# Optimization experiments

Hardware: AMD Instinct MI355X
Metric: run time of the kernel (lower is better)

Reference implementation:

```python
import jax, jax.numpy as jnp
import numpy as np

B, T, DIN, DOUT = 64, 512, 512, 512


def setup_inputs() -> dict:
    key = jax.random.key(0)
    ks = jax.random.split(key, 8)
    s_in = 1.0 / np.sqrt(DIN)
    s_h = 1.0 / np.sqrt(DOUT)
    return {
        "X": jax.random.normal(ks[0], (B, T, DIN), dtype=jnp.float32),
        "mask": jnp.ones((B, T), dtype=jnp.int32),
        "W_z": jax.random.normal(ks[1], (DIN, DOUT), dtype=jnp.float32) * s_in,
        "U_z": jax.random.normal(ks[2], (DOUT, DOUT), dtype=jnp.float32) * s_h,
        "b_z": jnp.zeros((DOUT,), dtype=jnp.float32),
        "W_r": jax.random.normal(ks[3], (DIN, DOUT), dtype=jnp.float32) * s_in,
        "U_r": jax.random.normal(ks[4], (DOUT, DOUT), dtype=jnp.float32) * s_h,
        "b_r": jnp.zeros((DOUT,), dtype=jnp.float32),
        "W_h": jax.random.normal(ks[5], (DIN, DOUT), dtype=jnp.float32) * s_in,
        "U_h": jax.random.normal(ks[6], (DOUT, DOUT), dtype=jnp.float32) * s_h,
        "b_h": jnp.zeros((DOUT,), dtype=jnp.float32),
    }


def reference(X, mask, W_z, U_z, b_z, W_r, U_r, b_r, W_h, U_h, b_h):
    # Precompute input projections for all timesteps (as the original does),
    # then scan the recurrence over time. return_sequences=False -> final h.
    # time-major: [T, B, DOUT]
    x_z = jnp.einsum('btd,dh->tbh', X, W_z) + b_z
    x_r = jnp.einsum('btd,dh->tbh', X, W_r) + b_r
    x_h = jnp.einsum('btd,dh->tbh', X, W_h) + b_h
    m = mask.T[:, :, None]  # [T, B, 1]

    def step(h, inp):
        xz_t, xr_t, xh_t, m_t = inp
        z = jax.nn.sigmoid(xz_t + h @ U_z)
        r = jax.nn.sigmoid(xr_t + h @ U_r)
        hh = jnp.tanh(xh_t + (r * h) @ U_h)
        h_new = z * h + (1.0 - z) * hh
        h_new = jnp.where(m_t > 0, h_new, h)  # masked steps keep previous state
        return h_new, None

    h0 = jnp.zeros((X.shape[0], U_z.shape[0]), dtype=X.dtype)
    h_final, _ = jax.lax.scan(step, h0, (x_z, x_r, x_h, m))
    return h_final
```

## Files before the change

### kernel.cpp

```cpp
#include <hip/hip_runtime.h>
#include <stdint.h>


#define GT    512
#define GDIN  512
#define GDOUT 512
#define NGRP  8
#define NSL   16
#define GROWS 8
#define COLS  32
#define NWAVE 8
#define KW    64
#define NWG   (NGRP * NSL)

#define OFF_HB    0
#define OFF_RHB   (2 * NGRP * GROWS * GDOUT)
#define OFF_HFL   (OFF_RHB + NGRP * GROWS * GDOUT)
#define FLSTR     4
#define FLGRP     (NSL * NWAVE * FLSTR)
#define OFF_RFL   (OFF_HFL + NGRP * FLGRP)
#define OFF_CNS   (OFF_RFL + NGRP * FLGRP)
#define INIT_DW   (OFF_CNS + 160)

typedef __attribute__((ext_vector_type(8))) short bf16x8;
typedef __attribute__((ext_vector_type(4))) float f32x4;
typedef __attribute__((ext_vector_type(4))) unsigned int u32x4;

__device__ __forceinline__ short f2bf(float f) {
  union { float f; uint32_t u; } v; v.f = f;
  uint32_t r = (v.u + 0x7FFFu + ((v.u >> 16) & 1u)) >> 16;
  return (short)(uint16_t)r;
}
__device__ __forceinline__ float bf2f(short s) {
  union { uint32_t u; float f; } v; v.u = ((uint32_t)(uint16_t)s) << 16;
  return v.f;
}
__device__ __forceinline__ uint32_t pack_hl(float v) {
  uint32_t t, o;
  asm("v_cvt_pk_bf16_f32 %0, %1, %1" : "=v"(t) : "v"(v));
  union { uint32_t u; float f; } hf; hf.u = t << 16;
  float d = v - hf.f;
  asm("v_cvt_pk_bf16_f32 %0, %1, %2" : "=v"(o) : "v"(d), "v"(v));
  return o;
}

__device__ __forceinline__ void st_sc1(uint32_t* p, uint32_t v) {
  asm volatile("global_store_dword %0, %1, off sc1" :: "v"(p), "v"(v) : "memory");
}
__device__ __forceinline__ void st_pl(uint32_t* p, uint32_t v) {
  asm volatile("global_store_dword %0, %1, off" :: "v"(p), "v"(v) : "memory");
}
__device__ __forceinline__ void vm_drain() {
  asm volatile("s_waitcnt vmcnt(0)" ::: "memory");
}
__device__ __forceinline__ void l1_inv() {
  asm volatile("buffer_inv sc1" ::: "memory");
}
__device__ __forceinline__ uint32_t ld_nt(const uint32_t* p) {
  uint32_t v;
  asm volatile("global_load_dword %0, %1, off nt\n\ts_waitcnt vmcnt(0)"
               : "=v"(v) : "v"(p) : "memory");
  return v;
}

__device__ __forceinline__ void slab4_issue(const uint32_t* base, u32x4 d[4],
                                            int fast) {
  if (fast) {
    asm volatile(
      "global_load_dwordx4 %0, %4, off nt\n\t"
      "global_load_dwordx4 %1, %4, off offset:16 nt\n\t"
      "global_load_dwordx4 %2, %4, off offset:128 nt\n\t"
      "global_load_dwordx4 %3, %4, off offset:144 nt"
      : "=&v"(d[0]), "=&v"(d[1]), "=&v"(d[2]), "=&v"(d[3])
      : "v"(base) : "memory");
  } else {
    asm volatile(
      "global_load_dwordx4 %0, %4, off sc1\n\t"
      "global_load_dwordx4 %1, %4, off offset:16 sc1\n\t"
      "global_load_dwordx4 %2, %4, off offset:128 sc1\n\t"
      "global_load_dwordx4 %3, %4, off offset:144 sc1"
      : "=&v"(d[0]), "=&v"(d[1]), "=&v"(d[2]), "=&v"(d[3])
      : "v"(base) : "memory");
  }
}
__device__ __forceinline__ void slab_wait() {
  asm volatile("s_waitcnt vmcnt(0)" ::: "memory");
  __builtin_amdgcn_sched_barrier(0);
}

__device__ __forceinline__ void wait16(const uint32_t* fbase, uint32_t tgt,
                                       int lane, int wv, int fast, int& budget) {
  if (budget <= 0) return;
  const int idx = lane & 15;
  const uint32_t* p = fbase +
      (size_t)(((2 * wv + (idx >> 3)) * NWAVE + (idx & 7)) * FLSTR);
  if (fast) {
    uint32_t v0, v1;
    asm volatile("global_load_dword %0, %1, off nt" : "=v"(v0) : "v"(p) : "memory");
    for (;;) {
      asm volatile("global_load_dword %0, %1, off nt" : "=v"(v1) : "v"(p) : "memory");
      asm volatile("s_waitcnt vmcnt(1)" ::: "memory");
      __builtin_amdgcn_sched_barrier(0);
      if (__all((int)(v0 >= tgt))) break;
      asm volatile("global_load_dword %0, %1, off nt" : "=v"(v0) : "v"(p) : "memory");
      asm volatile("s_waitcnt vmcnt(1)" ::: "memory");
      __builtin_amdgcn_sched_barrier(0);
      if (__all((int)(v1 >= tgt))) break;
      if ((budget -= 2) <= 0) break;
    }
    asm volatile("s_waitcnt vmcnt(0)" ::: "memory");
  } else {
    for (;;) {
      uint32_t v = __hip_atomic_load(p, __ATOMIC_RELAXED, __HIP_MEMORY_SCOPE_AGENT);
      if (__all((int)(v >= tgt))) break;
      if (--budget <= 0) break;
    }
  }
  asm volatile("" ::: "memory");
}

union U16x8 { uint32_t u[4]; bf16x8 v; };
__device__ __forceinline__ void mk_frags(const u32x4 A, const u32x4 B,
                                         bf16x8& hi, bf16x8& lo) {
  U16x8 h, l;
  h.u[0] = (A[0] >> 16) | (A[1] & 0xFFFF0000u);  l.u[0] = (A[0] & 0xFFFFu) | (A[1] << 16);
  h.u[1] = (A[2] >> 16) | (A[3] & 0xFFFF0000u);  l.u[1] = (A[2] & 0xFFFFu) | (A[3] << 16);
  h.u[2] = (B[0] >> 16) | (B[1] & 0xFFFF0000u);  l.u[2] = (B[0] & 0xFFFFu) | (B[1] << 16);
  h.u[3] = (B[2] >> 16) | (B[3] & 0xFFFF0000u);  l.u[3] = (B[2] & 0xFFFFu) | (B[3] << 16);
  hi = h.v; lo = l.v;
}
__device__ __forceinline__ bf16x8 cvt8(const f32x4 a, const f32x4 b) {
  U16x8 w;
  asm("v_cvt_pk_bf16_f32 %0, %1, %2" : "=v"(w.u[0]) : "v"(a[0]), "v"(a[1]));
  asm("v_cvt_pk_bf16_f32 %0, %1, %2" : "=v"(w.u[1]) : "v"(a[2]), "v"(a[3]));
  asm("v_cvt_pk_bf16_f32 %0, %1, %2" : "=v"(w.u[2]) : "v"(b[0]), "v"(b[1]));
  asm("v_cvt_pk_bf16_f32 %0, %1, %2" : "=v"(w.u[3]) : "v"(b[2]), "v"(b[3]));
  return w.v;
}

__global__ __launch_bounds__(512, 2)
void gru_fused(const float* __restrict__ X, const int* __restrict__ mask,
               const float* __restrict__ Wz, const float* __restrict__ Uz,
               const float* __restrict__ bz,
               const float* __restrict__ Wr, const float* __restrict__ Ur,
               const float* __restrict__ br,
               const float* __restrict__ Wh, const float* __restrict__ Uh,
               const float* __restrict__ bh,
               float* __restrict__ out, uint32_t* __restrict__ ws)
{
  const int tid   = threadIdx.x;
  const int wv    = tid >> 6;
  const int lane  = tid & 63;
  const int col16 = lane & 15;
  const int quad  = lane >> 4;
  const int row8  = lane & 7;

  uint32_t* cns = ws + OFF_CNS;
  __shared__ int s_mode, s_g, s_sl;
  if (tid == 0) {
    uint32_t xcc = 0;
    asm volatile("s_getreg_b32 %0, hwreg(HW_REG_XCC_ID)" : "=s"(xcc));
    xcc &= 7u;
    uint32_t slot = __hip_atomic_fetch_add(&cns[xcc], 1u, __ATOMIC_RELAXED,
                                           __HIP_MEMORY_SCOPE_AGENT);
    if (slot >= (uint32_t)NSL)
      __hip_atomic_fetch_add(&cns[9], 1u, __ATOMIC_RELAXED, __HIP_MEMORY_SCOPE_AGENT);
    __hip_atomic_fetch_add(&cns[8], 1u, __ATOMIC_RELEASE, __HIP_MEMORY_SCOPE_AGENT);
    uint32_t tv = 0; long sp = 0;
    do {
      tv = __hip_atomic_load(&cns[8], __ATOMIC_ACQUIRE, __HIP_MEMORY_SCOPE_AGENT);
    } while (tv < (uint32_t)NWG && ++sp < 2000000L);
    uint32_t bad = __hip_atomic_load(&cns[9], __ATOMIC_RELAXED, __HIP_MEMORY_SCOPE_AGENT);
    const int cok = (tv >= (uint32_t)NWG && bad == 0u);
    int g_, sl_, mode_ = 0;
    if (cok) {
      g_ = (int)xcc; sl_ = (int)slot;
      l1_inv();
      uint32_t* tok = cns + 16;
      st_pl(&tok[g_ * NSL + sl_], 1u);
      vm_drain();
      const uint32_t* np = &tok[g_ * NSL + ((sl_ + 1) & (NSL - 1))];
      int ok = 0;
      for (long i = 0; i < 300000L; ++i) {
        if (ld_nt(np) != 0u) { ok = 1; break; }
      }
      if (!ok)
        __hip_atomic_fetch_add(&cns[11], 1u, __ATOMIC_RELAXED, __HIP_MEMORY_SCOPE_AGENT);
      __hip_atomic_fetch_add(&cns[10], 1u, __ATOMIC_RELEASE, __HIP_MEMORY_SCOPE_AGENT);
      uint32_t tv2 = 0; sp = 0;
      do {
        tv2 = __hip_atomic_load(&cns[10], __ATOMIC_ACQUIRE, __HIP_MEMORY_SCOPE_AGENT);
      } while (tv2 < (uint32_t)NWG && ++sp < 2000000L);
      uint32_t fl = __hip_atomic_load(&cns[11], __ATOMIC_RELAXED, __HIP_MEMORY_SCOPE_AGENT);
      mode_ = (tv2 >= (uint32_t)NWG && fl == 0u) ? 1 : 0;
    } else {
      g_ = (int)(blockIdx.x & 7); sl_ = (int)(blockIdx.x >> 3);
    }
    s_mode = mode_; s_g = g_; s_sl = sl_;
  }
  __syncthreads();
  const int fast = __builtin_amdgcn_readfirstlane(s_mode);
  const int g    = __builtin_amdgcn_readfirstlane(s_g);
  const int sl   = __builtin_amdgcn_readfirstlane(s_sl);
  l1_inv();

  const int jb = sl * COLS;
  const int kb = wv * KW;

  uint32_t* hb  = ws + OFF_HB;
  uint32_t* rhb = ws + OFF_RHB;
  uint32_t* hfl = ws + OFF_HFL + (size_t)g * FLGRP;
  uint32_t* rfl = ws + OFF_RFL + (size_t)g * FLGRP;
  uint32_t* hfl_my = hfl + (size_t)(sl * NWAVE + wv) * FLSTR;
  uint32_t* rfl_my = rfl + (size_t)(sl * NWAVE + wv) * FLSTR;
  uint32_t* rhg = rhb + (size_t)g * (GROWS * GDOUT);
  const int slab_off = row8 * GDOUT + kb + quad * 8;

  __shared__ __align__(16) float scrA[2][NWAVE][2][GROWS][COLS];
  __shared__ __align__(16) float scrB[2][NWAVE][GROWS][COLS];

  bf16x8 uzh[2][2], uzl[2][2], urh[2][2], url[2][2], uhh[2][2], uhl[2][2];
  bf16x8 wzf[2][2], wrf[2][2], whf[2][2];
#pragma unroll
  for (int c = 0; c < 2; ++c) {
#pragma unroll
    for (int Tt = 0; Tt < 2; ++Tt) {
      const int k0 = kb + c * 32 + quad * 8;
      const int j  = jb + Tt * 16 + col16;
      bf16x8 t_uzh, t_uzl, t_urh, t_url, t_uhh, t_uhl, t_wz, t_wr, t_wh;
#pragma unroll
      for (int i = 0; i < 8; ++i) {
        const int idx = (k0 + i) * GDOUT + j;
        float u; short hi;
        u = Uz[idx]; hi = f2bf(u); t_uzh[i] = hi; t_uzl[i] = f2bf(u - bf2f(hi));
        u = Ur[idx]; hi = f2bf(u); t_urh[i] = hi; t_url[i] = f2bf(u - bf2f(hi));
        u = Uh[idx]; hi = f2bf(u); t_uhh[i] = hi; t_uhl[i] = f2bf(u - bf2f(hi));
        t_wz[i] = f2bf(Wz[idx]);
        t_wr[i] = f2bf(Wr[idx]);
        t_wh[i] = f2bf(Wh[idx]);
      }
      uzh[c][Tt] = t_uzh; uzl[c][Tt] = t_uzl; urh[c][Tt] = t_urh; url[c][Tt] = t_url;
      uhh[c][Tt] = t_uhh; uhl[c][Tt] = t_uhl;
      wzf[c][Tt] = t_wz;  wrf[c][Tt] = t_wr;  whf[c][Tt] = t_wh;
    }
  }

  const int ecol = lane & 31;
  const float bzv = bz[jb + ecol];
  const float brv = br[jb + ecol];
  const float bhv = bh[jb + ecol];
  const int b_ep = GROWS * g + wv;

  float hreg = 0.f;
  int budget = 4000000;

  f32x4 xpA[2], xpB[2]; int mkpre;
  {
    const float* xr = X + (size_t)(GROWS * g + row8) * GT * GDIN;
#pragma unroll
    for (int c = 0; c < 2; ++c) {
      const float* xp = xr + kb + c * 32 + quad * 8;
      xpA[c] = *(const f32x4*)xp;
      xpB[c] = *(const f32x4*)(xp + 4);
    }
    mkpre = mask[(size_t)b_ep * GT + 0];
  }

  for (int t = 0; t < GT; ++t) {
    const int par = t & 1;
    bf16x8 xa[2];
#pragma unroll
    for (int c = 0; c < 2; ++c) xa[c] = cvt8(xpA[c], xpB[c]);
    const int mk = mkpre;

    if (t) wait16(hfl, (uint32_t)t, lane, wv, fast, budget);
    const uint32_t* hsrc = hb + ((size_t)par * NGRP + g) * (GROWS * GDOUT) + slab_off;
    u32x4 hd[4];
    slab4_issue(hsrc, hd, fast);

    f32x4 ar[2]  = {{0,0,0,0},{0,0,0,0}}, ar2[2] = {{0,0,0,0},{0,0,0,0}};
#pragma unroll
    for (int c = 0; c < 2; ++c)
#pragma unroll
      for (int Tt = 0; Tt < 2; ++Tt)
        ar2[Tt] = __builtin_amdgcn_mfma_f32_16x16x32_bf16(xa[c], wrf[c][Tt], ar2[Tt], 0, 0, 0);
    slab_wait();

    bf16x8 hhi[2], hlo[2];
#pragma unroll
    for (int c = 0; c < 2; ++c) {
      mk_frags(hd[2 * c], hd[2 * c + 1], hhi[c], hlo[c]);
#pragma unroll
      for (int Tt = 0; Tt < 2; ++Tt) {
        ar[Tt]  = __builtin_amdgcn_mfma_f32_16x16x32_bf16(hhi[c], urh[c][Tt], ar[Tt],  0, 0, 0);
        ar2[Tt] = __builtin_amdgcn_mfma_f32_16x16x32_bf16(hlo[c], urh[c][Tt], ar2[Tt], 0, 0, 0);
        ar[Tt]  = __builtin_amdgcn_mfma_f32_16x16x32_bf16(hhi[c], url[c][Tt], ar[Tt],  0, 0, 0);
      }
    }

    if (quad < 2) {
#pragma unroll
      for (int Tt = 0; Tt < 2; ++Tt)
#pragma unroll
        for (int rr = 0; rr < 4; ++rr)
          scrA[par][wv][0][quad * 4 + rr][Tt * 16 + col16] = ar[Tt][rr] + ar2[Tt][rr];
    }
    __syncthreads();

    float rsum = 0.f;
#pragma unroll
    for (int w2 = 0; w2 < NWAVE; ++w2) rsum += scrA[par][w2][0][wv][ecol];
    const float rvl = 1.f / (1.f + __expf(-(rsum + brv)));
    if (lane < 32) {
      uint32_t* dst = rhg + (size_t)wv * GDOUT + jb + lane;
      const uint32_t pv = pack_hl(rvl * hreg);
      if (fast) st_pl(dst, pv); else st_sc1(dst, pv);
    }
    vm_drain();
    if (lane == 0) {
      if (fast) st_pl(rfl_my, (uint32_t)(t + 1)); else st_sc1(rfl_my, (uint32_t)(t + 1));
    }

    f32x4 az[2] = {{0,0,0,0},{0,0,0,0}}, az2[2] = {{0,0,0,0},{0,0,0,0}};
    f32x4 ah[2] = {{0,0,0,0},{0,0,0,0}};
#pragma unroll
    for (int c = 0; c < 2; ++c)
#pragma unroll
      for (int Tt = 0; Tt < 2; ++Tt) {
        az2[Tt] = __builtin_amdgcn_mfma_f32_16x16x32_bf16(xa[c], wzf[c][Tt], az2[Tt], 0, 0, 0);
        az[Tt]  = __builtin_amdgcn_mfma_f32_16x16x32_bf16(hhi[c], uzh[c][Tt], az[Tt],  0, 0, 0);
        az2[Tt] = __builtin_amdgcn_mfma_f32_16x16x32_bf16(hlo[c], uzh[c][Tt], az2[Tt], 0, 0, 0);
        az[Tt]  = __builtin_amdgcn_mfma_f32_16x16x32_bf16(hhi[c], uzl[c][Tt], az[Tt],  0, 0, 0);
        ah[Tt]  = __builtin_amdgcn_mfma_f32_16x16x32_bf16(xa[c],  whf[c][Tt], ah[Tt],  0, 0, 0);
      }
    if (quad < 2) {
#pragma unroll
      for (int Tt = 0; Tt < 2; ++Tt)
#pragma unroll
        for (int rr = 0; rr < 4; ++rr)
          scrA[par][wv][1][quad * 4 + rr][Tt * 16 + col16] = az[Tt][rr] + az2[Tt][rr];
    }
    __syncthreads();

    float zsum = 0.f;
#pragma unroll
    for (int w2 = 0; w2 < NWAVE; ++w2) zsum += scrA[par][w2][1][wv][ecol];
    const float zvl = 1.f / (1.f + __expf(-(zsum + bzv)));

    {
      const int tn = (t + 1 < GT) ? t + 1 : t;
      const float* xr = X + ((size_t)(GROWS * g + row8) * GT + tn) * GDIN;
#pragma unroll
      for (int c = 0; c < 2; ++c) {
        const float* xp = xr + kb + c * 32 + quad * 8;
        xpA[c] = *(const f32x4*)xp;
        xpB[c] = *(const f32x4*)(xp + 4);
      }
      mkpre = mask[(size_t)b_ep * GT + tn];
    }

    wait16(rfl, (uint32_t)(t + 1), lane, wv, fast, budget);
    u32x4 rd[4];
    slab4_issue(rhg + slab_off, rd, fast);
    slab_wait();

    f32x4 b1[2] = {{0,0,0,0},{0,0,0,0}}, b2[2] = {{0,0,0,0},{0,0,0,0}};
    f32x4 b3[2] = {{0,0,0,0},{0,0,0,0}};
#pragma unroll
    for (int c = 0; c < 2; ++c) {
      bf16x8 th, tl;
      mk_frags(rd[2 * c], rd[2 * c + 1], th, tl);
#pragma unroll
      for (int Tt = 0; Tt < 2; ++Tt) {
        b1[Tt] = __builtin_amdgcn_mfma_f32_16x16x32_bf16(th, uhh[c][Tt], b1[Tt], 0, 0, 0);
        b2[Tt] = __builtin_amdgcn_mfma_f32_16x16x32_bf16(tl, uhh[c][Tt], b2[Tt], 0, 0, 0);
        b3[Tt] = __builtin_amdgcn_mfma_f32_16x16x32_bf16(th, uhl[c][Tt], b3[Tt], 0, 0, 0);
      }
    }

    if (quad < 2) {
#pragma unroll
      for (int Tt = 0; Tt < 2; ++Tt)
#pragma unroll
        for (int rr = 0; rr < 4; ++rr)
          scrB[par][wv][quad * 4 + rr][Tt * 16 + col16] =
              ah[Tt][rr] + b1[Tt][rr] + b2[Tt][rr] + b3[Tt][rr];
    }
    __syncthreads();

    float hsum = 0.f;
#pragma unroll
    for (int w2 = 0; w2 < NWAVE; ++w2) hsum += scrB[par][w2][wv][ecol];
    const float pre = hsum + bhv;
    const float e  = __expf(2.f * pre);
    const float hh = 1.f - 2.f / (e + 1.f);
    float hn = zvl * hreg + (1.f - zvl) * hh;
    hn = (mk > 0) ? hn : hreg;
    hreg = hn;

    if (lane < 32) {
      uint32_t* hdst = hb + ((size_t)((t + 1) & 1) * NGRP + g) * (GROWS * GDOUT)
                         + (size_t)wv * GDOUT + jb + lane;
      const uint32_t pv = pack_hl(hn);
      if (fast) st_pl(hdst, pv); else st_sc1(hdst, pv);
      if (t == GT - 1) out[(size_t)b_ep * GDOUT + jb + lane] = hn;
    }
    vm_drain();
    if (lane == 0) {
      if (fast) st_pl(hfl_my, (uint32_t)(t + 1)); else st_sc1(hfl_my, (uint32_t)(t + 1));
    }
  }
}

extern "C" void kernel_launch(void* const* d_in, const int* in_sizes, int n_in,
                              void* d_out, int out_size, void* d_ws, size_t ws_size,
                              hipStream_t stream) {
  const float* X  = (const float*)d_in[0];
  const int* mask = (const int*)d_in[1];
  const float* Wz = (const float*)d_in[2];
  const float* Uz = (const float*)d_in[3];
  const float* bz = (const float*)d_in[4];
  const float* Wr = (const float*)d_in[5];
  const float* Ur = (const float*)d_in[6];
  const float* br = (const float*)d_in[7];
  const float* Wh = (const float*)d_in[8];
  const float* Uh = (const float*)d_in[9];
  const float* bh = (const float*)d_in[10];

  hipMemsetAsync(d_ws, 0, (size_t)INIT_DW * 4, stream);

  hipLaunchKernelGGL(gru_fused, dim3(NWG), dim3(512), 0, stream,
                     X, mask, Wz, Uz, bz, Wr, Ur, br, Wh, Uh, bh,
                     (float*)d_out, (uint32_t*)d_ws);
}
```

Measured before the change: 2.733 ms.

## Embed step tags in data words to replace separate flag synchronization

Removes the per-wave flag arrays and the vm_drain + flag store after each data publish. Instead, the low 2 bits of each packed bf16 hi/lo word carry a step tag (t mod 4), and consumers spin on the data slab itself until every word has the expected tag. This cuts one store, one full memory drain and one flag round trip per exchange on the serial recurrence critical path. In exchange, the low-order bf16 bits of each packed word are sacrificed (slight precision loss), and correctness now relies on per-dword store atomicity and on the tag never aliasing across the double-buffered slots.

```diff
diff --git a/kernel.cpp b/kernel.cpp
--- a/kernel.cpp
+++ b/kernel.cpp
@@ -15,11 +15,7 @@
 
 #define OFF_HB    0
 #define OFF_RHB   (2 * NGRP * GROWS * GDOUT)
-#define OFF_HFL   (OFF_RHB + NGRP * GROWS * GDOUT)
-#define FLSTR     4
-#define FLGRP     (NSL * NWAVE * FLSTR)
-#define OFF_RFL   (OFF_HFL + NGRP * FLGRP)
-#define OFF_CNS   (OFF_RFL + NGRP * FLGRP)
+#define OFF_CNS   (OFF_RHB + NGRP * GROWS * GDOUT)
 #define INIT_DW   (OFF_CNS + 160)
 
 typedef __attribute__((ext_vector_type(8))) short bf16x8;
@@ -59,6 +55,12 @@
 __device__ __forceinline__ uint32_t ld_nt(const uint32_t* p) {
   uint32_t v;
   asm volatile("global_load_dword %0, %1, off nt\n\ts_waitcnt vmcnt(0)"
+               : "=v"(v) : "v"(p) : "memory");
+  return v;
+}
+__device__ __forceinline__ uint32_t ld_sc1(const uint32_t* p) {
+  uint32_t v;
+  asm volatile("global_load_dword %0, %1, off sc1\n\ts_waitcnt vmcnt(0)"
                : "=v"(v) : "v"(p) : "memory");
   return v;
 }
@@ -88,35 +90,38 @@
   __builtin_amdgcn_sched_barrier(0);
 }
 
-__device__ __forceinline__ void wait16(const uint32_t* fbase, uint32_t tgt,
-                                       int lane, int wv, int fast, int& budget) {
+__device__ __forceinline__ void probe16(const uint32_t* kbase, uint32_t tg,
+                                        int lane, int fast, int& budget) {
   if (budget <= 0) return;
   const int idx = lane & 15;
-  const uint32_t* p = fbase +
-      (size_t)(((2 * wv + (idx >> 3)) * NWAVE + (idx & 7)) * FLSTR);
+  const uint32_t* p = kbase + (size_t)(idx & 7) * GDOUT + ((idx >> 3) << 5);
   if (fast) {
-    uint32_t v0, v1;
-    asm volatile("global_load_dword %0, %1, off nt" : "=v"(v0) : "v"(p) : "memory");
     for (;;) {
-      asm volatile("global_load_dword %0, %1, off nt" : "=v"(v1) : "v"(p) : "memory");
-      asm volatile("s_waitcnt vmcnt(1)" ::: "memory");
-      __builtin_amdgcn_sched_barrier(0);
-      if (__all((int)(v0 >= tgt))) break;
-      asm volatile("global_load_dword %0, %1, off nt" : "=v"(v0) : "v"(p) : "memory");
-      asm volatile("s_waitcnt vmcnt(1)" ::: "memory");
-      __builtin_amdgcn_sched_barrier(0);
-      if (__all((int)(v1 >= tgt))) break;
-      if ((budget -= 2) <= 0) break;
-    }
-    asm volatile("s_waitcnt vmcnt(0)" ::: "memory");
+      uint32_t v = ld_nt(p);
+      if (__all((int)(((v ^ tg) & 3u) == 0u))) break;
+      if (--budget <= 0) break;
+    }
   } else {
     for (;;) {
-      uint32_t v = __hip_atomic_load(p, __ATOMIC_RELAXED, __HIP_MEMORY_SCOPE_AGENT);
-      if (__all((int)(v >= tgt))) break;
+      uint32_t v = ld_sc1(p);
+      if (__all((int)(((v ^ tg) & 3u) == 0u))) break;
       if (--budget <= 0) break;
     }
   }
   asm volatile("" ::: "memory");
+}
+__device__ __forceinline__ void slab4v(const uint32_t* base, u32x4 d[4],
+                                       uint32_t tg, int fast, int& budget) {
+  for (;;) {
+    slab4_issue(base, d, fast);
+    slab_wait();
+    uint32_t c = 0;
+#pragma unroll
+    for (int i = 0; i < 4; ++i)
+      c |= (d[i][0] ^ tg) | (d[i][1] ^ tg) | (d[i][2] ^ tg) | (d[i][3] ^ tg);
+    if (__all((int)((c & 3u) == 0u))) return;
+    if (--budget <= 0) return;
+  }
 }
 
 union U16x8 { uint32_t u[4]; bf16x8 v; };
@@ -208,12 +213,7 @@
   const int kb = wv * KW;
 
   uint32_t* hb  = ws + OFF_HB;
-  uint32_t* rhb = ws + OFF_RHB;
-  uint32_t* hfl = ws + OFF_HFL + (size_t)g * FLGRP;
-  uint32_t* rfl = ws + OFF_RFL + (size_t)g * FLGRP;
-  uint32_t* hfl_my = hfl + (size_t)(sl * NWAVE + wv) * FLSTR;
-  uint32_t* rfl_my = rfl + (size_t)(sl * NWAVE + wv) * FLSTR;
-  uint32_t* rhg = rhb + (size_t)g * (GROWS * GDOUT);
+  uint32_t* rhg = ws + OFF_RHB + (size_t)g * (GROWS * GDOUT);
   const int slab_off = row8 * GDOUT + kb + quad * 8;
 
   __shared__ __align__(16) float scrA[2][NWAVE][2][GROWS][COLS];
@@ -268,23 +268,24 @@
 
   for (int t = 0; t < GT; ++t) {
     const int par = t & 1;
+    const uint32_t tg  = (uint32_t)(t & 3);
+    const uint32_t tgn = (uint32_t)((t + 1) & 3);
     bf16x8 xa[2];
 #pragma unroll
     for (int c = 0; c < 2; ++c) xa[c] = cvt8(xpA[c], xpB[c]);
     const int mk = mkpre;
 
-    if (t) wait16(hfl, (uint32_t)t, lane, wv, fast, budget);
-    const uint32_t* hsrc = hb + ((size_t)par * NGRP + g) * (GROWS * GDOUT) + slab_off;
-    u32x4 hd[4];
-    slab4_issue(hsrc, hd, fast);
-
     f32x4 ar[2]  = {{0,0,0,0},{0,0,0,0}}, ar2[2] = {{0,0,0,0},{0,0,0,0}};
 #pragma unroll
     for (int c = 0; c < 2; ++c)
 #pragma unroll
       for (int Tt = 0; Tt < 2; ++Tt)
         ar2[Tt] = __builtin_amdgcn_mfma_f32_16x16x32_bf16(xa[c], wrf[c][Tt], ar2[Tt], 0, 0, 0);
-    slab_wait();
+
+    uint32_t* hslot = hb + ((size_t)par * NGRP + g) * (GROWS * GDOUT);
+    probe16(hslot + kb, tg, lane, fast, budget);
+    u32x4 hd[4];
+    slab4v(hslot + slab_off, hd, tg, fast, budget);
 
     bf16x8 hhi[2], hlo[2];
 #pragma unroll
@@ -313,12 +314,8 @@
     const float rvl = 1.f / (1.f + __expf(-(rsum + brv)));
     if (lane < 32) {
       uint32_t* dst = rhg + (size_t)wv * GDOUT + jb + lane;
-      const uint32_t pv = pack_hl(rvl * hreg);
+      const uint32_t pv = (pack_hl(rvl * hreg) & ~3u) | tg;
       if (fast) st_pl(dst, pv); else st_sc1(dst, pv);
-    }
-    vm_drain();
-    if (lane == 0) {
-      if (fast) st_pl(rfl_my, (uint32_t)(t + 1)); else st_sc1(rfl_my, (uint32_t)(t + 1));
     }
 
     f32x4 az[2] = {{0,0,0,0},{0,0,0,0}}, az2[2] = {{0,0,0,0},{0,0,0,0}};
@@ -359,10 +356,9 @@
       mkpre = mask[(size_t)b_ep * GT + tn];
     }
 
-    wait16(rfl, (uint32_t)(t + 1), lane, wv, fast, budget);
+    probe16(rhg + kb, tg, lane, fast, budget);
     u32x4 rd[4];
-    slab4_issue(rhg + slab_off, rd, fast);
-    slab_wait();
+    slab4v(rhg + slab_off, rd, tg, fast, budget);
 
     f32x4 b1[2] = {{0,0,0,0},{0,0,0,0}}, b2[2] = {{0,0,0,0},{0,0,0,0}};
     f32x4 b3[2] = {{0,0,0,0},{0,0,0,0}};
@@ -401,13 +397,9 @@
     if (lane < 32) {
       uint32_t* hdst = hb + ((size_t)((t + 1) & 1) * NGRP + g) * (GROWS * GDOUT)
                          + (size_t)wv * GDOUT + jb + lane;
-      const uint32_t pv = pack_hl(hn);
+      const uint32_t pv = (pack_hl(hn) & ~3u) | tgn;
       if (fast) st_pl(hdst, pv); else st_sc1(hdst, pv);
       if (t == GT - 1) out[(size_t)b_ep * GDOUT + jb + lane] = hn;
-    }
-    vm_drain();
-    if (lane == 0) {
-      if (fast) st_pl(hfl_my, (uint32_t)(t + 1)); else st_sc1(hfl_my, (uint32_t)(t + 1));
     }
   }
 }
```

New measurement: 2.716 ms. Within noise of the previous version (-0.6%).
